# Kernel optimization log

Measured on AMD Instinct MI355X. Metric: run time of the kernel, lower is better.

Reference implementation:

```python
import jax, jax.numpy as jnp
import numpy as np

H = 1024

def setup_inputs() -> dict:
    key = jax.random.key(0)
    k1, k2, k3, k4, k5 = jax.random.split(key, 5)
    B, T = 32, 2048
    s = 1.0 / np.sqrt(H)
    return {
        "decoder_state": jax.random.normal(k1, (B, H), dtype=jnp.float32),
        "encoder_states": jax.random.normal(k2, (B, T, H), dtype=jnp.float32),
        "Wa_w": jax.random.uniform(k3, (H, H), jnp.float32, -s, s),
        "Wa_b": jnp.zeros((H,), jnp.float32),
        "Ua_w": jax.random.uniform(k4, (H, H), jnp.float32, -s, s),
        "Ua_b": jnp.zeros((H,), jnp.float32),
        "v_w": jax.random.uniform(k5, (H,), jnp.float32, -s, s),
        "v_b": jnp.zeros((), jnp.float32),
    }

def reference(decoder_state, encoder_states, Wa_w, Wa_b, Ua_w, Ua_b, v_w, v_b):
    # decoder_state: [B,H], encoder_states: [B,T,H]
    dec_proj = decoder_state @ Ua_w.T + Ua_b            # [B,H]
    enc_proj = jnp.einsum('bth,oh->bto', encoder_states, Wa_w) + Wa_b  # [B,T,H]
    e = jnp.tanh(dec_proj[:, None, :] + enc_proj)        # [B,T,H]
    scores = jnp.einsum('bth,h->bt', e, v_w) + v_b       # [B,T]
    attn_weights = jax.nn.softmax(scores, axis=1)        # [B,T]
    context = jnp.einsum('bt,bth->bh', attn_weights, encoder_states)  # [B,H]
    return (context, attn_weights)
```

## Files before the change

### kernel.cpp

```cpp
#include <hip/hip_runtime.h>
#include <hip/hip_bf16.h>

#define HH 1024
#define BB 32
#define TT 2048

typedef __attribute__((ext_vector_type(8))) short bf16x8;
typedef __attribute__((ext_vector_type(4))) float f32x4;

static __device__ __forceinline__ unsigned short f2bf(float f) {
    unsigned int u = __float_as_uint(f);
    unsigned int r = u + 0x7fffu + ((u >> 16) & 1u);
    return (unsigned short)(r >> 16);
}
static __device__ __forceinline__ unsigned int cvt_pk_bf16(float lo, float hi) {
    unsigned int d;
    asm volatile("v_cvt_pk_bf16_f32 %0, %1, %2" : "=v"(d) : "v"(lo), "v"(hi));
    return d;
}
static __device__ __forceinline__ float fast_tanh(float x) {
    float e = __expf(2.0f * x);
    return 1.0f - 2.0f / (e + 1.0f);
}

#define GLOAD_LDS16(gp, lp) \
    __builtin_amdgcn_global_load_lds( \
        (const __attribute__((address_space(1))) void*)(gp), \
        (__attribute__((address_space(3))) void*)(lp), 16, 0, 0)

__global__ void k_convW(const float* __restrict__ W, unsigned short* __restrict__ Wb) {
    int i = blockIdx.x * 256 + threadIdx.x;
    float4 v = ((const float4*)W)[i];
    ushort4 o;
    o.x = f2bf(v.x); o.y = f2bf(v.y); o.z = f2bf(v.z); o.w = f2bf(v.w);
    ((ushort4*)Wb)[i] = o;
}

__global__ void k_decproj(const float* __restrict__ dec, const float* __restrict__ Ua,
                          const float* __restrict__ Uab, const float* __restrict__ Wab,
                          float* __restrict__ dp) {
    int gtid = blockIdx.x * 256 + threadIdx.x;
    int b = gtid >> 10, o = gtid & 1023;
    const float4* d4 = (const float4*)(dec + (long)b * HH);
    const float4* u4 = (const float4*)(Ua + (long)o * HH);
    float acc = 0.f;
    for (int k = 0; k < HH / 4; ++k) {
        float4 a = d4[k], w = u4[k];
        acc += a.x * w.x + a.y * w.y + a.z * w.z + a.w * w.w;
    }
    dp[gtid] = acc + Uab[o] + Wab[o];
}

__global__ __launch_bounds__(512) void k_score_bf(
        const float* __restrict__ enc, const unsigned short* __restrict__ Wb,
        const float* __restrict__ dp, const float* __restrict__ vw,
        float* __restrict__ scores) {
    __shared__ __align__(16) unsigned short As[2][256 * 64];
    __shared__ __align__(16) unsigned short Bs[2][256 * 64];
    int bid = blockIdx.x;
    int xcd = bid & 7;
    int ord = bid >> 3;
    int nt = ord & 3;
    int mt = (ord >> 2) * 8 + xcd;
    long m0 = (long)mt * 256;
    int o0b = nt * 256;
    int tid = threadIdx.x;
    int lane = tid & 63, wid = tid >> 6;
    int wm = wid >> 2, wn = wid & 3;
    int r = lane & 15, g = lane >> 4;

    f32x4 acc[8][4];
    #pragma unroll
    for (int i = 0; i < 8; ++i)
        #pragma unroll
        for (int j = 0; j < 4; ++j) acc[i][j] = (f32x4){0.f, 0.f, 0.f, 0.f};

    int srow = tid >> 3;
    int acol = (tid & 7) * 8;
    int awu = (tid & 7) ^ (srow & 7);
    int swu = awu;
    const float* aSrcF = enc + (m0 + srow) * HH + acol;
    const unsigned short* bSrc = Wb + (long)(o0b + srow) * HH + swu * 8;
    int ldso = wid * 512;
    int rx = r & 7;
    int u0 = (g ^ rx) * 8;
    int u1 = ((4 + g) ^ rx) * 8;

    int aw0 = srow * 64 + awu * 8;

    {
        float4 ar[8];
        #pragma unroll
        for (int q = 0; q < 4; ++q) {
            ar[2 * q]     = *(const float4*)(aSrcF + (long)64 * q * HH);
            ar[2 * q + 1] = *(const float4*)(aSrcF + (long)64 * q * HH + 4);
            GLOAD_LDS16(bSrc + (long)q * 64 * HH, &Bs[0][ldso + q * 4096]);
        }
        #pragma unroll
        for (int q = 0; q < 4; ++q) {
            uint4 w;
            w.x = cvt_pk_bf16(ar[2 * q].x, ar[2 * q].y);
            w.y = cvt_pk_bf16(ar[2 * q].z, ar[2 * q].w);
            w.z = cvt_pk_bf16(ar[2 * q + 1].x, ar[2 * q + 1].y);
            w.w = cvt_pk_bf16(ar[2 * q + 1].z, ar[2 * q + 1].w);
            *(uint4*)(&As[0][aw0 + q * 4096]) = w;
        }
    }
    __syncthreads();

    #pragma unroll 1
    for (int t = 0; t < 16; ++t) {
        int bi = t & 1, pi = bi ^ 1;
        int kc2 = (t + 1) * 64;
        bool pre = (t < 15);
        float4 ar[8];

        bf16x8 bfr[4][2];
        #pragma unroll
        for (int ni = 0; ni < 4; ++ni) {
            int rowb = (wn * 64 + ni * 16 + r) * 64;
            bfr[ni][0] = *(const bf16x8*)(&Bs[bi][rowb + u0]);
            bfr[ni][1] = *(const bf16x8*)(&Bs[bi][rowb + u1]);
        }
        bf16x8 aq[2][2][2];
        #pragma unroll
        for (int q = 0; q < 2; ++q) {
            int rowa = (wm * 128 + q * 16 + r) * 64;
            aq[0][q][0] = *(const bf16x8*)(&As[bi][rowa + u0]);
            aq[0][q][1] = *(const bf16x8*)(&As[bi][rowa + u1]);
        }

        #pragma unroll
        for (int p = 0; p < 4; ++p) {
            if (pre && p == 0) {
                #pragma unroll
                for (int q = 0; q < 4; ++q) {
                    ar[2 * q]     = *(const float4*)(aSrcF + (long)64 * q * HH + kc2);
                    ar[2 * q + 1] = *(const float4*)(aSrcF + (long)64 * q * HH + kc2 + 4);
                }
                GLOAD_LDS16(bSrc + kc2 + (long)0 * 64 * HH, &Bs[pi][ldso + 0 * 4096]);
                GLOAD_LDS16(bSrc + kc2 + (long)1 * 64 * HH, &Bs[pi][ldso + 1 * 4096]);
            }
            if (pre && p == 1) {
                GLOAD_LDS16(bSrc + kc2 + (long)2 * 64 * HH, &Bs[pi][ldso + 2 * 4096]);
                GLOAD_LDS16(bSrc + kc2 + (long)3 * 64 * HH, &Bs[pi][ldso + 3 * 4096]);
            }
            if (p < 3) {
                #pragma unroll
                for (int q = 0; q < 2; ++q) {
                    int rowa = (wm * 128 + (2 * (p + 1) + q) * 16 + r) * 64;
                    aq[(p + 1) & 1][q][0] = *(const bf16x8*)(&As[bi][rowa + u0]);
                    aq[(p + 1) & 1][q][1] = *(const bf16x8*)(&As[bi][rowa + u1]);
                }
            }
            __builtin_amdgcn_s_setprio(1);
            #pragma unroll
            for (int q = 0; q < 2; ++q) {
                int mi = 2 * p + q;
                #pragma unroll
                for (int ni = 0; ni < 4; ++ni) {
                    acc[mi][ni] = __builtin_amdgcn_mfma_f32_16x16x32_bf16(
                        aq[p & 1][q][0], bfr[ni][0], acc[mi][ni], 0, 0, 0);
                    acc[mi][ni] = __builtin_amdgcn_mfma_f32_16x16x32_bf16(
                        aq[p & 1][q][1], bfr[ni][1], acc[mi][ni], 0, 0, 0);
                }
            }
            __builtin_amdgcn_s_setprio(0);
        }
        if (pre) {
            #pragma unroll
            for (int q = 0; q < 4; ++q) {
                uint4 w;
                w.x = cvt_pk_bf16(ar[2 * q].x, ar[2 * q].y);
                w.y = cvt_pk_bf16(ar[2 * q].z, ar[2 * q].w);
                w.z = cvt_pk_bf16(ar[2 * q + 1].x, ar[2 * q + 1].y);
                w.w = cvt_pk_bf16(ar[2 * q + 1].z, ar[2 * q + 1].w);
                *(uint4*)(&As[pi][aw0 + q * 4096]) = w;
            }
        }
        __syncthreads();
    }

    int bb = (int)(m0 >> 11);
    float vv[4], dpv[4];
    #pragma unroll
    for (int ni = 0; ni < 4; ++ni) {
        int o = o0b + wn * 64 + ni * 16 + r;
        vv[ni] = vw[o];
        dpv[ni] = dp[bb * HH + o];
    }
    #pragma unroll
    for (int mi = 0; mi < 8; ++mi) {
        float vp[4] = {0.f, 0.f, 0.f, 0.f};
        #pragma unroll
        for (int ni = 0; ni < 4; ++ni)
            #pragma unroll
            for (int j = 0; j < 4; ++j)
                vp[j] += fast_tanh(acc[mi][ni][j] + dpv[ni]) * vv[ni];
        #pragma unroll
        for (int j = 0; j < 4; ++j) {
            float s = vp[j];
            s += __shfl_xor(s, 1); s += __shfl_xor(s, 2);
            s += __shfl_xor(s, 4); s += __shfl_xor(s, 8);
            if (r == 0) {
                int row = wm * 128 + mi * 16 + g * 4 + j;
                atomicAdd(&scores[m0 + row], s);
            }
        }
    }
}

__global__ void k_softmax(float* __restrict__ w) {
    int b = blockIdx.x;
    float* row = w + (long)b * TT;
    int tid = threadIdx.x;
    float loc[8];
    float m = -1e30f;
    #pragma unroll
    for (int i = 0; i < 8; ++i) { loc[i] = row[tid + i * 256]; m = fmaxf(m, loc[i]); }
    #pragma unroll
    for (int off = 1; off < 64; off <<= 1) m = fmaxf(m, __shfl_xor(m, off));
    __shared__ float red[4];
    if ((tid & 63) == 0) red[tid >> 6] = m;
    __syncthreads();
    m = fmaxf(fmaxf(red[0], red[1]), fmaxf(red[2], red[3]));
    float s = 0.f;
    #pragma unroll
    for (int i = 0; i < 8; ++i) { loc[i] = __expf(loc[i] - m); s += loc[i]; }
    #pragma unroll
    for (int off = 1; off < 64; off <<= 1) s += __shfl_xor(s, off);
    __shared__ float red2[4];
    if ((tid & 63) == 0) red2[tid >> 6] = s;
    __syncthreads();
    s = red2[0] + red2[1] + red2[2] + red2[3];
    float inv = 1.0f / s;
    #pragma unroll
    for (int i = 0; i < 8; ++i) row[tid + i * 256] = loc[i] * inv;
}

__global__ void k_context(const float* __restrict__ enc, const float* __restrict__ w,
                          float* __restrict__ ctx) {
    int bid = blockIdx.x;
    int b = bid >> 6;
    int hc = (bid >> 4) & 3;
    int ts = bid & 15;
    int h = hc * 256 + threadIdx.x;
    const float* wr = w + (long)b * TT + ts * 128;
    long base = ((long)b * TT + (long)ts * 128) * HH + h;
    float acc = 0.f;
    #pragma unroll 4
    for (int t = 0; t < 128; ++t)
        acc += wr[t] * enc[base + (long)t * HH];
    atomicAdd(&ctx[b * HH + h], acc);
}

extern "C" void kernel_launch(void* const* d_in, const int* in_sizes, int n_in,
                              void* d_out, int out_size, void* d_ws, size_t ws_size,
                              hipStream_t stream) {
    const float* dec  = (const float*)d_in[0];
    const float* enc  = (const float*)d_in[1];
    const float* Wa_w = (const float*)d_in[2];
    const float* Wa_b = (const float*)d_in[3];
    const float* Ua_w = (const float*)d_in[4];
    const float* Ua_b = (const float*)d_in[5];
    const float* v_w  = (const float*)d_in[6];

    float* out  = (float*)d_out;
    float* ctx  = out;
    float* attn = out + BB * HH;

    float* dpw = (float*)d_ws;
    unsigned short* Wb = (unsigned short*)((char*)d_ws + 131072);

    hipMemsetAsync(d_out, 0, (size_t)out_size * sizeof(float), stream);
    k_convW<<<1024, 256, 0, stream>>>(Wa_w, Wb);
    k_decproj<<<128, 256, 0, stream>>>(dec, Ua_w, Ua_b, Wa_b, dpw);
    k_score_bf<<<1024, 512, 0, stream>>>(enc, Wb, dpw, v_w, attn);
    k_softmax<<<BB, 256, 0, stream>>>(attn);
    k_context<<<2048, 256, 0, stream>>>(enc, attn, ctx);
}
```

Measured before the change: 265.1 us.

## Prefetch fp32 encoder tiles two stages ahead with manual waitcnt barriers

Moves the global register loads of the fp32 encoder A-tile from the start of each k-step to the end of the previous step, so they are issued two iterations ahead and overlap a full step of MFMA work. __syncthreads is replaced with explicit s_waitcnt vmcnt/lgkmcnt plus s_barrier, so only the older loads are waited on. The aim is to hide HBM latency on the A operand. The cost is manual counter bookkeeping that must stay correct.

Result: no change. 262.3 us, median of 2 (-1.1%).

```diff
diff --git a/kernel.cpp b/kernel.cpp
--- a/kernel.cpp
+++ b/kernel.cpp
@@ -78,42 +78,49 @@
     int srow = tid >> 3;
     int acol = (tid & 7) * 8;
     int awu = (tid & 7) ^ (srow & 7);
-    int swu = awu;
     const float* aSrcF = enc + (m0 + srow) * HH + acol;
-    const unsigned short* bSrc = Wb + (long)(o0b + srow) * HH + swu * 8;
+    const unsigned short* bSrc = Wb + (long)(o0b + srow) * HH + awu * 8;
     int ldso = wid * 512;
     int rx = r & 7;
     int u0 = (g ^ rx) * 8;
     int u1 = ((4 + g) ^ rx) * 8;
-
     int aw0 = srow * 64 + awu * 8;
 
+    float4 ar[8];
+
     {
-        float4 ar[8];
+        float4 a0[8];
         #pragma unroll
         for (int q = 0; q < 4; ++q) {
-            ar[2 * q]     = *(const float4*)(aSrcF + (long)64 * q * HH);
-            ar[2 * q + 1] = *(const float4*)(aSrcF + (long)64 * q * HH + 4);
+            a0[2 * q]     = *(const float4*)(aSrcF + (long)64 * q * HH);
+            a0[2 * q + 1] = *(const float4*)(aSrcF + (long)64 * q * HH + 4);
             GLOAD_LDS16(bSrc + (long)q * 64 * HH, &Bs[0][ldso + q * 4096]);
         }
         #pragma unroll
         for (int q = 0; q < 4; ++q) {
             uint4 w;
-            w.x = cvt_pk_bf16(ar[2 * q].x, ar[2 * q].y);
-            w.y = cvt_pk_bf16(ar[2 * q].z, ar[2 * q].w);
-            w.z = cvt_pk_bf16(ar[2 * q + 1].x, ar[2 * q + 1].y);
-            w.w = cvt_pk_bf16(ar[2 * q + 1].z, ar[2 * q + 1].w);
+            w.x = cvt_pk_bf16(a0[2 * q].x, a0[2 * q].y);
+            w.y = cvt_pk_bf16(a0[2 * q].z, a0[2 * q].w);
+            w.z = cvt_pk_bf16(a0[2 * q + 1].x, a0[2 * q + 1].y);
+            w.w = cvt_pk_bf16(a0[2 * q + 1].z, a0[2 * q + 1].w);
             *(uint4*)(&As[0][aw0 + q * 4096]) = w;
         }
-    }
-    __syncthreads();
+        #pragma unroll
+        for (int q = 0; q < 4; ++q) {
+            ar[2 * q]     = *(const float4*)(aSrcF + (long)64 * q * HH + 64);
+            ar[2 * q + 1] = *(const float4*)(aSrcF + (long)64 * q * HH + 64 + 4);
+        }
+        asm volatile("s_waitcnt vmcnt(8)" ::: "memory");
+        asm volatile("s_waitcnt lgkmcnt(0)" ::: "memory");
+        __builtin_amdgcn_s_barrier();
+        __builtin_amdgcn_sched_barrier(0);
+    }
 
     #pragma unroll 1
     for (int t = 0; t < 16; ++t) {
         int bi = t & 1, pi = bi ^ 1;
         int kc2 = (t + 1) * 64;
         bool pre = (t < 15);
-        float4 ar[8];
 
         bf16x8 bfr[4][2];
         #pragma unroll
@@ -133,11 +140,6 @@
         #pragma unroll
         for (int p = 0; p < 4; ++p) {
             if (pre && p == 0) {
-                #pragma unroll
-                for (int q = 0; q < 4; ++q) {
-                    ar[2 * q]     = *(const float4*)(aSrcF + (long)64 * q * HH + kc2);
-                    ar[2 * q + 1] = *(const float4*)(aSrcF + (long)64 * q * HH + kc2 + 4);
-                }
                 GLOAD_LDS16(bSrc + kc2 + (long)0 * 64 * HH, &Bs[pi][ldso + 0 * 4096]);
                 GLOAD_LDS16(bSrc + kc2 + (long)1 * 64 * HH, &Bs[pi][ldso + 1 * 4096]);
             }
@@ -167,6 +169,7 @@
             }
             __builtin_amdgcn_s_setprio(0);
         }
+
         if (pre) {
             #pragma unroll
             for (int q = 0; q < 4; ++q) {
@@ -178,7 +181,22 @@
                 *(uint4*)(&As[pi][aw0 + q * 4096]) = w;
             }
         }
-        __syncthreads();
+        if (t < 14) {
+            int kc3 = (t + 2) * 64;
+            #pragma unroll
+            for (int q = 0; q < 4; ++q) {
+                ar[2 * q]     = *(const float4*)(aSrcF + (long)64 * q * HH + kc3);
+                ar[2 * q + 1] = *(const float4*)(aSrcF + (long)64 * q * HH + kc3 + 4);
+            }
+            asm volatile("s_waitcnt vmcnt(8)" ::: "memory");
+        } else if (t == 14) {
+            asm volatile("s_waitcnt vmcnt(0)" ::: "memory");
+        }
+        if (pre) {
+            asm volatile("s_waitcnt lgkmcnt(0)" ::: "memory");
+            __builtin_amdgcn_s_barrier();
+            __builtin_amdgcn_sched_barrier(0);
+        }
     }
 
     int bb = (int)(m0 >> 11);
```
